# Kernel optimization log

Measured on AMD Instinct MI355X. Metric: run time of the kernel, lower is better.

Reference implementation:

```python
import jax, jax.numpy as jnp
import numpy as np

N = 100_000      # nodes
E = 400_000      # edges
POS = 3          # pos_dim
F = 128          # feats_dim (kernel_dim)
M = 16           # m_dim
FE = 16          # fourier_features
EIN = 2 * F + 2 * FE + 1   # 289 edge mlp input
EHID = 2 * EIN             # 578
NIN = F + M                # 144
NHID = 2 * F               # 256
EPS = 1e-5


def _ln(x, g, b):
    m = x.mean(-1, keepdims=True)
    v = ((x - m) ** 2).mean(-1, keepdims=True)
    return (x - m) * jax.lax.rsqrt(v + EPS) * g + b


def setup_inputs() -> dict:
    key = jax.random.key(0)
    ks = jax.random.split(key, 8)

    def xav(k, i, o):
        return jax.random.normal(k, (i, o), jnp.float32) * np.float32(np.sqrt(2.0 / (i + o)))

    x = jax.random.normal(ks[0], (N, POS + F), jnp.float32)
    edge_index = jax.random.randint(ks[1], (2, E), 0, N, dtype=jnp.int64)
    return {
        "x": x,
        "edge_index": edge_index,
        "e_w1": xav(ks[2], EIN, EHID), "e_b1": jnp.zeros((EHID,), jnp.float32),
        "e_w2": xav(ks[3], EHID, M),   "e_b2": jnp.zeros((M,), jnp.float32),
        "en1_g": jnp.ones((M,), jnp.float32), "en1_b": jnp.zeros((M,), jnp.float32),
        "en2_g": jnp.ones((M,), jnp.float32), "en2_b": jnp.zeros((M,), jnp.float32),
        "nn1_g": jnp.ones((F,), jnp.float32), "nn1_b": jnp.zeros((F,), jnp.float32),
        "n_w1": xav(ks[4], NIN, NHID), "n_b1": jnp.zeros((NHID,), jnp.float32),
        "n_w2": xav(ks[5], NHID, F),   "n_b2": jnp.zeros((F,), jnp.float32),
        "nn2_g": jnp.ones((F,), jnp.float32), "nn2_b": jnp.zeros((F,), jnp.float32),
    }


def reference(x, edge_index, e_w1, e_b1, e_w2, e_b2, en1_g, en1_b, en2_g, en2_b,
              nn1_g, nn1_b, n_w1, n_b1, n_w2, n_b2, nn2_g, nn2_b):
    coors, feats = x[:, :POS], x[:, POS:]
    src, dst = edge_index[0], edge_index[1]  # x_j = feats[src], x_i = feats[dst]

    rel = coors[src] - coors[dst]                      # [E,3]
    d = (rel ** 2).sum(-1, keepdims=True)              # [E,1] squared distance
    scales = jnp.asarray(2.0, jnp.float32) ** jnp.arange(FE)
    ds = d / scales                                    # [E,FE]
    edge_attr = jnp.concatenate([jnp.sin(ds), jnp.cos(ds), d], -1)  # [E,2*FE+1]

    # edge MLP + LayerNorm (message)
    m = jnp.concatenate([feats[dst], feats[src], edge_attr], -1)    # [E,EIN]
    m = jax.nn.silu(m @ e_w1 + e_b1)
    m = jax.nn.silu(m @ e_w2 + e_b2)                                # [E,M]
    m = _ln(m, en1_g, en1_b)

    # scatter-add to target nodes, then LayerNorm
    m_i = jax.ops.segment_sum(m, dst, num_segments=N)               # [N,M]
    m_i = _ln(m_i, en2_g, en2_b)

    # node update MLP with residual
    h = jnp.concatenate([_ln(feats, nn1_g, nn1_b), m_i], -1)        # [N,NIN]
    h = jax.nn.silu(h @ n_w1 + n_b1)
    h = h @ n_w2 + n_b2
    h = _ln(h, nn2_g, nn2_b)
    out = feats + h
    return jnp.concatenate([coors, out], -1)                        # [N,POS+F]
```

## Files before the change

### kernel.cpp

```cpp
#include <hip/hip_runtime.h>
#include <math.h>

#define N_NODES 100000
#define N_EDGES 400000
#define POSD 3
#define F 128
#define M 16
#define EIN 289
#define EHID 578
#define NIN 144
#define NHID 256
#define ROW 131
#define LNEPS 1e-5f

#define KP 320
#define NP 640
#define EPB 32
#define NSLICE 10
#define NTW 5
#define HIDP 640

#define NPB2 80
#define NK1 160
#define NK1P 168
#define NSL2 5
#define NHIDP 264

typedef _Float16 half8 __attribute__((ext_vector_type(8)));
typedef _Float16 half4 __attribute__((ext_vector_type(4)));
typedef float f32x4 __attribute__((ext_vector_type(4)));

__device__ __forceinline__ float silu_f(float v) { return v / (1.f + __expf(-v)); }

__global__ __launch_bounds__(256) void prep_feats(
    const float* __restrict__ x, _Float16* __restrict__ feats)
{
    long long i = (long long)blockIdx.x * 256 + threadIdx.x;
    if (i < (long long)N_NODES * F) {
        int n = (int)(i >> 7), k = (int)(i & 127);
        feats[i] = (_Float16)x[(long long)n * ROW + POSD + k];
    }
}

__global__ __launch_bounds__(256) void prep_weights(
    const float* __restrict__ w1, const float* __restrict__ w2,
    _Float16* __restrict__ w1ks, _Float16* __restrict__ w2t)
{
    long long idx = (long long)blockIdx.x * 256 + threadIdx.x;
    const long long n1 = (long long)NSLICE * NP * 32;
    if (idx < n1) {
        int s   = (int)(idx / (NP * 32));
        int rem = (int)(idx - (long long)s * (NP * 32));
        int c   = rem >> 5;
        int kk  = rem & 31;
        int k   = s * 32 + kk;
        float v = (k < EIN && c < EHID) ? w1[(long long)k * EHID + c] : 0.f;
        w1ks[idx] = (_Float16)v;
    } else {
        long long j = idx - n1;
        if (j < (long long)M * HIDP) {
            int oc = (int)(j / HIDP);
            int k  = (int)(j - (long long)oc * HIDP);
            float v = (k < EHID) ? w2[(long long)k * M + oc] : 0.f;
            w2t[j] = (_Float16)v;
        }
    }
}

__global__ __launch_bounds__(256) void prep_weights_node(
    const float* __restrict__ w1, const float* __restrict__ w2,
    _Float16* __restrict__ w1ks2, _Float16* __restrict__ w2ks)
{
    int idx = blockIdx.x * 256 + threadIdx.x;
    const int n1 = NSL2 * 256 * 32;
    if (idx < n1) {
        int s = idx >> 13, rem = idx & 8191;
        int c = rem >> 5, kk = rem & 31;
        int k = s * 32 + kk;
        w1ks2[idx] = (_Float16)((k < NIN) ? w1[k * NHID + c] : 0.f);
    } else if (idx < n1 + 8 * 128 * 32) {
        int j = idx - n1;
        int s = j >> 12, rem = j & 4095;
        int c = rem >> 5, kk = rem & 31;
        int k = s * 32 + kk;
        w2ks[j] = (_Float16)w2[k * F + c];
    }
}

__global__ __launch_bounds__(512, 4) void edge_kernel(
    const _Float16* __restrict__ feats, const float* __restrict__ x,
    const int* __restrict__ ei,
    const _Float16* __restrict__ w1ks, const float* __restrict__ b1,
    const _Float16* __restrict__ w2t, const float* __restrict__ b2,
    const float* __restrict__ g1, const float* __restrict__ bb1,
    float* __restrict__ m_i)
{
    __shared__ __align__(16) _Float16 smem[EPB * HIDP];
    _Float16* lds_A = smem;
    _Float16* lds_H = smem;
    __shared__ int   src_s[EPB], dst_s[EPB];
    __shared__ float d_s[EPB];

    const int t    = threadIdx.x;
    const int lane = t & 63;
    const int wv   = t >> 6;
    const int cl16 = lane & 15;
    const int h4   = lane >> 4;
    const long long ebase = (long long)blockIdx.x * EPB;

    if (t < EPB) {
        int s = ei[ebase + t];
        int d = ei[(long long)N_EDGES + ebase + t];
        src_s[t] = s; dst_s[t] = d;
        float dx = x[(long long)s*ROW+0] - x[(long long)d*ROW+0];
        float dy = x[(long long)s*ROW+1] - x[(long long)d*ROW+1];
        float dz = x[(long long)s*ROW+2] - x[(long long)d*ROW+2];
        d_s[t] = dx*dx + dy*dy + dz*dz;
    }
    __syncthreads();

    for (int i = t; i < EPB * 32; i += 512) {
        int row = i >> 5, g = i & 31;
        int node = (g < 16) ? dst_s[row] : src_s[row];
        half8 v = *(const half8*)(feats + (long long)node * F + ((g & 15) << 3));
        *(half8*)(lds_A + row * KP + ((g ^ (row & 7)) << 3)) = v;
    }
    for (int i = t; i < EPB * 64; i += 512) {
        int row = i >> 6, j = i & 63;
        float v;
        if (j < 16)       v = __sinf(ldexpf(d_s[row], -j));
        else if (j < 32)  v = __cosf(ldexpf(d_s[row], -(j - 16)));
        else if (j == 32) v = d_s[row];
        else              v = 0.f;
        int g = 32 + (j >> 3);
        lds_A[row * KP + ((g ^ (row & 7)) << 3) + (j & 7)] = (_Float16)v;
    }
    __syncthreads();

    f32x4 acc[2][NTW] = {};
    #pragma unroll
    for (int s = 0; s < NSLICE; ++s) {
        half8 bf[NTW];
        #pragma unroll
        for (int nt = 0; nt < NTW; ++nt) {
            int ntile = wv * NTW + nt;
            bf[nt] = *(const half8*)(w1ks + (long long)s * (NP * 32)
                                     + ntile * 512 + cl16 * 32 + h4 * 8);
        }
        const int G = s * 4 + h4;
        const int aoff = ((G & ~7) | ((G ^ (cl16 & 7)) & 7)) << 3;
        half8 af[2];
        #pragma unroll
        for (int mt = 0; mt < 2; ++mt)
            af[mt] = *(const half8*)(lds_A + (mt * 16 + cl16) * KP + aoff);
        #pragma unroll
        for (int nt = 0; nt < NTW; ++nt) {
            #pragma unroll
            for (int mt = 0; mt < 2; ++mt)
                acc[mt][nt] = __builtin_amdgcn_mfma_f32_16x16x32_f16(
                                  af[mt], bf[nt], acc[mt][nt], 0, 0, 0);
        }
    }
    __syncthreads();

    #pragma unroll
    for (int nt = 0; nt < NTW; ++nt) {
        int hcol = (wv * NTW + nt) * 16 + cl16;
        float bias = (hcol < EHID) ? b1[hcol] : 0.f;
        int gcol = hcol >> 3;
        #pragma unroll
        for (int mt = 0; mt < 2; ++mt) {
            #pragma unroll
            for (int r = 0; r < 4; ++r) {
                int edge = mt * 16 + h4 * 4 + r;
                float v = (hcol < EHID) ? silu_f(acc[mt][nt][r] + bias) : 0.f;
                lds_H[edge * HIDP + (((gcol & ~7) | ((gcol ^ edge) & 7)) << 3) + (hcol & 7)]
                    = (_Float16)v;
            }
        }
    }
    __syncthreads();

    if (wv < 2) {
        f32x4 acc2 = {};
        const int oc = cl16;
        const int edgeA = wv * 16 + oc;
        #pragma unroll
        for (int ks = 0; ks < 20; ++ks) {
            int G2 = ks * 4 + h4;
            const half8 a = *(const half8*)(lds_H + edgeA * HIDP +
                               (((G2 & ~7) | ((G2 ^ edgeA) & 7)) << 3));
            const half8 b = *(const half8*)(w2t + oc * HIDP + ks * 32 + h4 * 8);
            acc2 = __builtin_amdgcn_mfma_f32_16x16x32_f16(a, b, acc2, 0, 0, 0);
        }
        float g = g1[oc], bb = bb1[oc], b2v = b2[oc];
        #pragma unroll
        for (int r = 0; r < 4; ++r) {
            int edge = wv * 16 + h4 * 4 + r;
            float v = silu_f(acc2[r] + b2v);
            float s = v, s2 = v * v;
            #pragma unroll
            for (int m = 8; m >= 1; m >>= 1) {
                s  += __shfl_xor(s,  m, 16);
                s2 += __shfl_xor(s2, m, 16);
            }
            float mean = s * (1.f / 16.f);
            float var  = s2 * (1.f / 16.f) - mean * mean;
            float outv = (v - mean) * rsqrtf(var + LNEPS) * g + bb;
            atomicAdd(&m_i[(long long)dst_s[edge] * M + oc], outv);
        }
    }
}

__global__ __launch_bounds__(512, 4) void node_kernel(
    const _Float16* __restrict__ feats, const float* __restrict__ x,
    const float* __restrict__ m_i,
    const float* __restrict__ en2g, const float* __restrict__ en2b,
    const float* __restrict__ nn1g, const float* __restrict__ nn1b,
    const _Float16* __restrict__ w1ks2, const float* __restrict__ b1,
    const _Float16* __restrict__ w2ks, const float* __restrict__ b2,
    const float* __restrict__ nn2g, const float* __restrict__ nn2b,
    float* __restrict__ out)
{
    __shared__ __align__(16) _Float16 smem[NPB2 * NHIDP];
    _Float16* lds_A = smem;
    _Float16* lds_H = smem;
    __shared__ float rsum2[NPB2], rsq2[NPB2];

    const int t    = threadIdx.x;
    const int lane = t & 63;
    const int wv   = t >> 6;
    const int cl16 = lane & 15;
    const int h4   = lane >> 4;
    const long long nb = (long long)blockIdx.x * NPB2;

    if (t < NPB2) { rsum2[t] = 0.f; rsq2[t] = 0.f; }

    #pragma unroll
    for (int p = 0; p < 5; ++p) {
        int nl = p * 16 + (t >> 5);
        int l  = t & 31;
        half4 v4 = *(const half4*)(feats + (nb + nl) * F + l * 4);
        float v[4]; float s = 0.f, s2 = 0.f;
        #pragma unroll
        for (int i = 0; i < 4; ++i) {
            v[i] = (float)v4[i]; s += v[i]; s2 += v[i]*v[i];
        }
        #pragma unroll
        for (int m = 16; m >= 1; m >>= 1) {
            s  += __shfl_xor(s,  m, 32);
            s2 += __shfl_xor(s2, m, 32);
        }
        float mean = s * (1.f/128.f);
        float var  = s2 * (1.f/128.f) - mean*mean;
        float rs   = rsqrtf(var + LNEPS);
        half4 w;
        #pragma unroll
        for (int i = 0; i < 4; ++i) {
            int c = l * 4 + i;
            w[i] = (_Float16)((v[i] - mean) * rs * nn1g[c] + nn1b[c]);
        }
        *(half4*)(lds_A + nl * NK1P + l * 4) = w;
    }
    for (int i = t; i < NPB2 * M; i += 512) {
        int nl = i >> 4, oc = i & 15;
        float v = m_i[(nb + nl) * M + oc];
        float a = v, a2 = v * v;
        #pragma unroll
        for (int m = 8; m >= 1; m >>= 1) {
            a  += __shfl_xor(a,  m, 16);
            a2 += __shfl_xor(a2, m, 16);
        }
        float mn = a * (1.f/16.f);
        float vr = a2 * (1.f/16.f) - mn*mn;
        float lv = (v - mn) * rsqrtf(vr + LNEPS) * en2g[oc] + en2b[oc];
        lds_A[nl * NK1P + 128 + oc] = (_Float16)lv;
    }
    for (int i = t; i < NPB2 * 16; i += 512) {
        int nl = i >> 4, j = i & 15;
        lds_A[nl * NK1P + 144 + j] = (_Float16)0.f;
    }
    __syncthreads();

    f32x4 acc[5][2] = {};
    #pragma unroll
    for (int s = 0; s < NSL2; ++s) {
        half8 bf[2];
        #pragma unroll
        for (int nt = 0; nt < 2; ++nt) {
            int ntile = wv * 2 + nt;
            bf[nt] = *(const half8*)(w1ks2 + s * (NHID * 32)
                                     + ntile * 512 + cl16 * 32 + h4 * 8);
        }
        const int G = s * 4 + h4;
        half8 af[5];
        #pragma unroll
        for (int mt = 0; mt < 5; ++mt)
            af[mt] = *(const half8*)(lds_A + (mt * 16 + cl16) * NK1P + G * 8);
        #pragma unroll
        for (int nt = 0; nt < 2; ++nt) {
            #pragma unroll
            for (int mt = 0; mt < 5; ++mt)
                acc[mt][nt] = __builtin_amdgcn_mfma_f32_16x16x32_f16(
                                  af[mt], bf[nt], acc[mt][nt], 0, 0, 0);
        }
    }
    __syncthreads();

    #pragma unroll
    for (int nt = 0; nt < 2; ++nt) {
        int hcol = (wv * 2 + nt) * 16 + cl16;
        float bias = b1[hcol];
        #pragma unroll
        for (int mt = 0; mt < 5; ++mt) {
            #pragma unroll
            for (int r = 0; r < 4; ++r) {
                int row = mt * 16 + h4 * 4 + r;
                float v = silu_f(acc[mt][nt][r] + bias);
                lds_H[row * NHIDP + hcol] = (_Float16)v;
            }
        }
    }
    __syncthreads();

    f32x4 acc2[5] = {};
    const int col = wv * 16 + cl16;
    #pragma unroll
    for (int s = 0; s < 8; ++s) {
        const half8 b = *(const half8*)(w2ks + s * (F * 32) + col * 32 + h4 * 8);
        const int G2 = s * 4 + h4;
        #pragma unroll
        for (int mt = 0; mt < 5; ++mt) {
            int row = mt * 16 + cl16;
            const half8 a = *(const half8*)(lds_H + row * NHIDP + G2 * 8);
            acc2[mt] = __builtin_amdgcn_mfma_f32_16x16x32_f16(a, b, acc2[mt], 0, 0, 0);
        }
    }

    float y[5][4];
    float b2v = b2[col];
    #pragma unroll
    for (int mt = 0; mt < 5; ++mt) {
        #pragma unroll
        for (int r = 0; r < 4; ++r) {
            float v = acc2[mt][r] + b2v;
            y[mt][r] = v;
            float s = v, s2 = v * v;
            #pragma unroll
            for (int m = 8; m >= 1; m >>= 1) {
                s  += __shfl_xor(s,  m, 16);
                s2 += __shfl_xor(s2, m, 16);
            }
            if (cl16 == 0) {
                int row = mt * 16 + h4 * 4 + r;
                atomicAdd(&rsum2[row], s);
                atomicAdd(&rsq2[row],  s2);
            }
        }
    }
    __syncthreads();

    float gcol2 = nn2g[col], bcol2 = nn2b[col];
    #pragma unroll
    for (int mt = 0; mt < 5; ++mt) {
        #pragma unroll
        for (int r = 0; r < 4; ++r) {
            int row = mt * 16 + h4 * 4 + r;
            long long node = nb + row;
            float mn = rsum2[row] * (1.f/128.f);
            float vr = rsq2[row] * (1.f/128.f) - mn*mn;
            float rs = rsqrtf(vr + LNEPS);
            float res = x[node * ROW + POSD + col];
            out[node * ROW + POSD + col] = res + (y[mt][r] - mn) * rs * gcol2 + bcol2;
        }
    }
    for (int i = t; i < NPB2 * POSD; i += 512) {
        int nl = i / 3, c = i - nl * 3;
        long long node = nb + nl;
        out[node * ROW + c] = x[node * ROW + c];
    }
}

extern "C" void kernel_launch(void* const* d_in, const int* in_sizes, int n_in,
                              void* d_out, int out_size, void* d_ws, size_t ws_size,
                              hipStream_t stream) {
    const float* x    = (const float*)d_in[0];
    const int*   ei   = (const int*)d_in[1];
    const float* e_w1 = (const float*)d_in[2];
    const float* e_b1 = (const float*)d_in[3];
    const float* e_w2 = (const float*)d_in[4];
    const float* e_b2 = (const float*)d_in[5];
    const float* en1g = (const float*)d_in[6];
    const float* en1b = (const float*)d_in[7];
    const float* en2g = (const float*)d_in[8];
    const float* en2b = (const float*)d_in[9];
    const float* nn1g = (const float*)d_in[10];
    const float* nn1b = (const float*)d_in[11];
    const float* n_w1 = (const float*)d_in[12];
    const float* n_b1 = (const float*)d_in[13];
    const float* n_w2 = (const float*)d_in[14];
    const float* n_b2 = (const float*)d_in[15];
    const float* nn2g = (const float*)d_in[16];
    const float* nn2b = (const float*)d_in[17];
    float* out = (float*)d_out;

    char* ws = (char*)d_ws;
    float*    m_i   = (float*)ws;
    _Float16* w1ks  = (_Float16*)(ws + 6400000);
    _Float16* w2t   = (_Float16*)(ws + 6809600);
    _Float16* feats = (_Float16*)(ws + 6830080);
    _Float16* w1ks2 = (_Float16*)(ws + 32430080);
    _Float16* w2ks  = (_Float16*)(ws + 32512000);

    hipMemsetAsync(m_i, 0, (size_t)N_NODES * M * sizeof(float), stream);
    prep_weights<<<840, 256, 0, stream>>>(e_w1, e_w2, w1ks, w2t);
    prep_weights_node<<<288, 256, 0, stream>>>(n_w1, n_w2, w1ks2, w2ks);
    prep_feats<<<(N_NODES * F + 255) / 256, 256, 0, stream>>>(x, feats);
    edge_kernel<<<N_EDGES / EPB, 512, 0, stream>>>(
        feats, x, ei, w1ks, e_b1, w2t, e_b2, en1g, en1b, m_i);
    node_kernel<<<N_NODES / NPB2, 512, 0, stream>>>(
        feats, x, m_i, en2g, en2b, nn1g, nn1b, w1ks2, n_b1, w2ks, n_b2, nn2g, nn2b, out);
}
```

Measured before the change: 565.9 us.

## Double-buffer edge W1 fragment loads and split second GEMM K across all waves

The first edge GEMM now prefetches the next K-slice's weight fragments into alternating register buffers, so global loads overlap with the MFMAs of the current slice. The second GEMM (hidden to M) previously ran on only 2 of 8 waves. It now splits the K dimension four ways across all 8 waves, writes partial sums to a new shared array, and reduces them after an extra barrier. This adds register pressure from the doubled B fragments, plus extra LDS and a sync, which could affect occupancy at 4 blocks per CU.

```diff
diff --git a/kernel.cpp b/kernel.cpp
--- a/kernel.cpp
+++ b/kernel.cpp
@@ -98,6 +98,7 @@
     __shared__ __align__(16) _Float16 smem[EPB * HIDP];
     _Float16* lds_A = smem;
     _Float16* lds_H = smem;
+    __shared__ float part[4][EPB][M];
     __shared__ int   src_s[EPB], dst_s[EPB];
     __shared__ float d_s[EPB];
 
@@ -138,14 +139,24 @@
     __syncthreads();
 
     f32x4 acc[2][NTW] = {};
-    #pragma unroll
-    for (int s = 0; s < NSLICE; ++s) {
-        half8 bf[NTW];
+    half8 bfA[NTW], bfB[NTW];
+    {
         #pragma unroll
         for (int nt = 0; nt < NTW; ++nt) {
             int ntile = wv * NTW + nt;
-            bf[nt] = *(const half8*)(w1ks + (long long)s * (NP * 32)
-                                     + ntile * 512 + cl16 * 32 + h4 * 8);
+            bfA[nt] = *(const half8*)(w1ks + ntile * 512 + cl16 * 32 + h4 * 8);
+        }
+    }
+    #pragma unroll
+    for (int s = 0; s < NSLICE; ++s) {
+        if (s + 1 < NSLICE) {
+            const _Float16* base = w1ks + (long long)(s + 1) * (NP * 32);
+            #pragma unroll
+            for (int nt = 0; nt < NTW; ++nt) {
+                int ntile = wv * NTW + nt;
+                half8 v = *(const half8*)(base + ntile * 512 + cl16 * 32 + h4 * 8);
+                if (s & 1) bfA[nt] = v; else bfB[nt] = v;
+            }
         }
         const int G = s * 4 + h4;
         const int aoff = ((G & ~7) | ((G ^ (cl16 & 7)) & 7)) << 3;
@@ -155,10 +166,11 @@
             af[mt] = *(const half8*)(lds_A + (mt * 16 + cl16) * KP + aoff);
         #pragma unroll
         for (int nt = 0; nt < NTW; ++nt) {
+            half8 b = (s & 1) ? bfB[nt] : bfA[nt];
             #pragma unroll
             for (int mt = 0; mt < 2; ++mt)
                 acc[mt][nt] = __builtin_amdgcn_mfma_f32_16x16x32_f16(
-                                  af[mt], bf[nt], acc[mt][nt], 0, 0, 0);
+                                  af[mt], b, acc[mt][nt], 0, 0, 0);
         }
     }
     __syncthreads();
@@ -181,23 +193,37 @@
     }
     __syncthreads();
 
-    if (wv < 2) {
+    {
+        const int eh = wv & 1;
+        const int kq = wv >> 1;
         f32x4 acc2 = {};
         const int oc = cl16;
-        const int edgeA = wv * 16 + oc;
-        #pragma unroll
-        for (int ks = 0; ks < 20; ++ks) {
+        const int edgeA = eh * 16 + oc;
+        #pragma unroll
+        for (int k5 = 0; k5 < 5; ++k5) {
+            int ks = kq * 5 + k5;
             int G2 = ks * 4 + h4;
             const half8 a = *(const half8*)(lds_H + edgeA * HIDP +
                                (((G2 & ~7) | ((G2 ^ edgeA) & 7)) << 3));
             const half8 b = *(const half8*)(w2t + oc * HIDP + ks * 32 + h4 * 8);
             acc2 = __builtin_amdgcn_mfma_f32_16x16x32_f16(a, b, acc2, 0, 0, 0);
         }
+        #pragma unroll
+        for (int r = 0; r < 4; ++r)
+            part[kq][eh * 16 + h4 * 4 + r][oc] = acc2[r];
+    }
+    __syncthreads();
+
+    if (wv < 2) {
+        const int eh = wv;
+        const int oc = cl16;
         float g = g1[oc], bb = bb1[oc], b2v = b2[oc];
         #pragma unroll
         for (int r = 0; r < 4; ++r) {
-            int edge = wv * 16 + h4 * 4 + r;
-            float v = silu_f(acc2[r] + b2v);
+            int edge = eh * 16 + h4 * 4 + r;
+            float v = part[0][edge][oc] + part[1][edge][oc]
+                    + part[2][edge][oc] + part[3][edge][oc] + b2v;
+            v = silu_f(v);
             float s = v, s2 = v * v;
             #pragma unroll
             for (int m = 8; m >= 1; m >>= 1) {
```

After: 572.1 us. Within noise of the previous version (+1.1%).
